# Optimization experiments

Measured on AMD Instinct MI355X. Metric: run time of the kernel, lower is better.

The kernel has to match this reference:

```python
import jax, jax.numpy as jnp
import numpy as np

N = 1024                      # FFT length (init kwarg)
NF = N // 2 + 1               # rfft output length = len(freq)
PB_LO = 40.0 / 60.0           # pulse_band[0] in Hz
PB_HI = 180.0 / 60.0          # pulse_band[1] in Hz
DELTA_HZ = 6.0 / 60.0         # self.delta after /60
W0, W1 = 1.0, 1.0             # weights[0], weights[1]
B, T = 32768, 1024


def setup_inputs() -> dict:
    key = jax.random.key(0)
    k1, k2 = jax.random.split(key)
    preds = jax.random.normal(k1, (B, T), dtype=jnp.float32)
    # realistic camera frame rates ~25-35 Hz (must exceed 2*pulse_band[1]=6 Hz)
    Fs = 25.0 + 10.0 * jax.random.uniform(k2, (B,), dtype=jnp.float32)
    return {"preds": preds, "Fs": Fs}


def reference(preds, Fs):
    idx = jnp.arange(NF)                                            # [Nf]
    # freq = linspace(0, Fs/2, Nf) per sample -> [B, Nf]
    freq = (Fs[:, None] * 0.5) * (idx.astype(jnp.float32) / (NF - 1))
    left = jnp.argmin(jnp.abs(freq - PB_LO), axis=1)                # [B] int
    right = jnp.argmin(jnp.abs(freq - PB_HI), axis=1)               # [B] int

    psd = jnp.abs(jnp.fft.rfft(preds, n=N)) ** 2                    # [B, Nf]
    total = jnp.sum(psd, axis=-1)                                   # [B]

    l = left[:, None]
    r = right[:, None]
    out_band = (idx < l) | (idx >= r)                               # psd[:left] + psd[right:]
    band_loss = jnp.sum(jnp.where(out_band, psd, 0.0), axis=-1) / (1e-8 + total)

    in_band = (idx >= l) & (idx < r)
    # argmax(psd[left:right]) + left  (psd >= 0, so -inf mask is safe)
    peak = jnp.argmax(jnp.where(in_band, psd, -jnp.inf), axis=1)    # [B]
    # delta = max(1, round(self.delta / (Fs/2/len(freq))))  (round half-to-even, as Python)
    delta = jnp.maximum(1.0, jnp.round(DELTA_HZ / (Fs * 0.5 / NF))).astype(jnp.int32)

    p = peak[:, None]
    d = delta[:, None]
    # psd[left:peak-delta] + psd[peak+delta:right]  (empty slices -> 0 via mask)
    sparse_mask = in_band & ((idx < p - d) | (idx >= p + d))
    num = jnp.sum(jnp.where(sparse_mask, psd, 0.0), axis=-1)
    # sum(psd[left:right] + 1e-8) adds 1e-8 per in-band bin, keep faithful
    den = jnp.sum(jnp.where(in_band, psd + 1e-8, 0.0), axis=-1)
    sparse_loss = num / den

    return W0 * jnp.mean(band_loss) + W1 * jnp.mean(sparse_loss)
```

## Files before the change

kernel.cpp:

```cpp
#include <hip/hip_runtime.h>
#include <cmath>

#define BATCH 32768
#define SROW  66

typedef float v2f __attribute__((ext_vector_type(2)));

__device__ __forceinline__ v2f mkc(float r, float i) { v2f t; t.x = r; t.y = i; return t; }
__device__ __forceinline__ v2f cmul(v2f a, v2f b) {
    v2f s = mkc(-a.y, a.x);
    return a * b.x + s * b.y;
}
__device__ __forceinline__ v2f cmul_mi(v2f a){ return mkc(a.y, -a.x); }
__device__ __forceinline__ v2f cmul_w81(v2f a){ const float C=0.70710678f; return mkc(C*(a.x+a.y), C*(a.y-a.x)); }
__device__ __forceinline__ v2f cmul_w83(v2f a){ const float C=0.70710678f; return mkc(C*(a.y-a.x), -C*(a.x+a.y)); }

__device__ __forceinline__ void dft8(v2f a[8]) {
    v2f t0=a[0]+a[4], t4=a[0]-a[4];
    v2f t1=a[1]+a[5], t5=a[1]-a[5];
    v2f t2=a[2]+a[6], t6=a[2]-a[6];
    v2f t3=a[3]+a[7], t7=a[3]-a[7];
    v2f u0=t0+t2, u2=t0-t2;
    v2f u1=t1+t3, u3=cmul_mi(t1-t3);
    a[0]=u0+u1; a[4]=u0-u1; a[2]=u2+u3; a[6]=u2-u3;
    v2f v0=t4, v1=cmul_w81(t5), v2=cmul_mi(t6), v3=cmul_w83(t7);
    v2f w0=v0+v2, w2=v0-v2;
    v2f w1=v1+v3, w3=cmul_mi(v1-v3);
    a[1]=w0+w1; a[5]=w0-w1; a[3]=w2+w3; a[7]=w2-w3;
}

__device__ __forceinline__ float wave_sum64(float x) {
    x += __int_as_float(__builtin_amdgcn_update_dpp(0, __float_as_int(x), 0x111, 0xf, 0xf, true));
    x += __int_as_float(__builtin_amdgcn_update_dpp(0, __float_as_int(x), 0x112, 0xf, 0xf, true));
    x += __int_as_float(__builtin_amdgcn_update_dpp(0, __float_as_int(x), 0x114, 0xf, 0xf, true));
    x += __int_as_float(__builtin_amdgcn_update_dpp(0, __float_as_int(x), 0x118, 0xf, 0xf, true));
    x += __int_as_float(__builtin_amdgcn_update_dpp(0, __float_as_int(x), 0x142, 0xf, 0xf, true));
    x += __int_as_float(__builtin_amdgcn_update_dpp(0, __float_as_int(x), 0x143, 0xf, 0xf, true));
    return __int_as_float(__builtin_amdgcn_readlane(__float_as_int(x), 63));
}
__device__ __forceinline__ int wave_argmax64(float best, int besti) {
#define AM_STEP(ctrl) { \
    float ob = __int_as_float(__builtin_amdgcn_update_dpp(__float_as_int(best), __float_as_int(best), ctrl, 0xf, 0xf, false)); \
    int   oi = __builtin_amdgcn_update_dpp(besti, besti, ctrl, 0xf, 0xf, false); \
    if (ob > best || (ob == best && oi < besti)) { best = ob; besti = oi; } }
    AM_STEP(0x111) AM_STEP(0x112) AM_STEP(0x114) AM_STEP(0x118) AM_STEP(0x142) AM_STEP(0x143)
#undef AM_STEP
    return __builtin_amdgcn_readlane(besti, 63);
}

__device__ __forceinline__ int nearest_bin(float fs, float target) {
    float x = target * 1024.0f / fs;
    int i0 = (int)floorf(x);
    int lo = max(0, i0 - 1), hi = min(512, i0 + 2);
    int bi = lo; float bd = 1e30f;
    for (int i = lo; i <= hi; ++i) {
        float fr = (fs * 0.5f) * ((float)i / 512.0f);
        float d = fabsf(fr - target);
        if (d < bd) { bd = d; bi = i; }
    }
    return bi;
}

__global__ __launch_bounds__(128, 5) void fft_loss_kernel(
    const float* __restrict__ preds, const float* __restrict__ Fs,
    float* __restrict__ wavepartial)
{
    __shared__ v2f lds[2][2][8 * SROW];

    const int tid  = threadIdx.x;
    const int wv   = tid >> 6;
    const int lane = tid & 63;
    const int row0 = blockIdx.x * 4 + wv * 2;

    v2f (*sm)[8 * SROW] = lds[wv];
    const v2f* x2 = reinterpret_cast<const v2f*>(preds) + (size_t)row0 * 512;

    const float fs_[2] = {Fs[row0], Fs[row0 + 1]};
    int left_[2], right_[2];
#pragma unroll
    for (int rr = 0; rr < 2; ++rr) {
        left_[rr]  = nearest_bin(fs_[rr], (float)(40.0 / 60.0));
        right_[rr] = nearest_bin(fs_[rr], 3.0f);
    }

    v2f z[2][8];
    v2f sacc[2]  = {mkc(0.f,0.f), mkc(0.f,0.f)};
    v2f ssacc[2] = {mkc(0.f,0.f), mkc(0.f,0.f)};
#pragma unroll
    for (int rr = 0; rr < 2; ++rr)
#pragma unroll
        for (int n1 = 0; n1 < 8; ++n1) {
            v2f v = x2[rr * 512 + n1 * 64 + lane];
            z[rr][n1] = v;
            sacc[rr]  += v;
            ssacc[rr] += v * v;
        }

    {
        float sb, cb;
        __sincosf(-0.012271846f * (float)lane, &sb, &cb);
        v2f w1 = mkc(cb, sb);
        v2f w2 = cmul(w1, w1), w3 = cmul(w2, w1), w4 = cmul(w2, w2);
        v2f w5 = cmul(w3, w2), w6 = cmul(w3, w3), w7 = cmul(w4, w3);
#pragma unroll
        for (int rr = 0; rr < 2; ++rr) {
            dft8(z[rr]);
            z[rr][1]=cmul(z[rr][1],w1); z[rr][2]=cmul(z[rr][2],w2); z[rr][3]=cmul(z[rr][3],w3);
            z[rr][4]=cmul(z[rr][4],w4); z[rr][5]=cmul(z[rr][5],w5); z[rr][6]=cmul(z[rr][6],w6);
            z[rr][7]=cmul(z[rr][7],w7);
#pragma unroll
            for (int r = 0; r < 8; ++r) sm[rr][r * SROW + lane] = z[rr][r];
        }
    }

    const int rB = lane & 7, m0 = lane >> 3;
    {
        float sb, cb;
        __sincosf(-0.09817477f * (float)m0, &sb, &cb);
        v2f b1 = mkc(cb, sb);
        v2f b2 = cmul(b1, b1), b3 = cmul(b2, b1), b4 = cmul(b2, b2);
        v2f b5 = cmul(b3, b2), b6 = cmul(b3, b3), b7 = cmul(b4, b3);
#pragma unroll
        for (int rr = 0; rr < 2; ++rr) {
#pragma unroll
            for (int m1 = 0; m1 < 8; ++m1) z[rr][m1] = sm[rr][rB * SROW + 8 * m1 + m0];
            dft8(z[rr]);
            z[rr][1]=cmul(z[rr][1],b1); z[rr][2]=cmul(z[rr][2],b2); z[rr][3]=cmul(z[rr][3],b3);
            z[rr][4]=cmul(z[rr][4],b4); z[rr][5]=cmul(z[rr][5],b5); z[rr][6]=cmul(z[rr][6],b6);
            z[rr][7]=cmul(z[rr][7],b7);
#pragma unroll
            for (int s = 0; s < 8; ++s)
                sm[rr][rB * SROW + 8 * m0 + ((s + m0) & 7)] = z[rr][s];
        }
    }

    const int sC = lane >> 3;
#pragma unroll
    for (int rr = 0; rr < 2; ++rr) {
#pragma unroll
        for (int m = 0; m < 8; ++m) z[rr][m] = sm[rr][rB * SROW + 8 * m + ((sC + m) & 7)];
        dft8(z[rr]);
    }

    const int pl = (64 - lane) & 63;
    float wk0x, wk0y;
    {
        float sk, ck;
        __sincosf(-0.0061359233f * (float)lane, &sk, &ck);
        wk0x = ck; wk0y = sk;
    }
    const float W16C = 0.99518473f, W16S = -0.098017140f;

    float acc = 0.f;
#pragma unroll
    for (int rr = 0; rr < 2; ++rr) {
        const int left = left_[rr], right = right_[rr];
        float psd[2];
        float inb = 0.f, best = -1.f;
        int besti = 1 << 30;
#pragma unroll
        for (int t = 0; t < 2; ++t) {
            v2f a = z[rr][t];
            float px = __shfl(z[rr][7 - t].x, pl);
            float py = __shfl(z[rr][7 - t].y, pl);
            if (lane == 0) { px = z[rr][(8 - t) & 7].x; py = z[rr][(8 - t) & 7].y; }
            float wkx = (t == 0) ? wk0x : wk0x * 0.92387953f - wk0y * (-0.38268343f);
            float wky = (t == 0) ? wk0y : wk0x * (-0.38268343f) + wk0y * 0.92387953f;
            float ex = 0.5f * (a.x + px), ey = 0.5f * (a.y - py);
            float dx = a.x - px,          dy = a.y + py;
            float ox = 0.5f * dy,         oy = -0.5f * dx;
            float Xr = ex + wkx * ox - wky * oy;
            float Xi = ey + wkx * oy + wky * ox;
            float v  = Xr * Xr + Xi * Xi;
            psd[t] = v;
            int k = lane + 64 * t;
            if (k >= left && k < right) {
                inb += v;
                if (v > best) { best = v; besti = k; }
            }
        }

        float Se = wave_sum64(sacc[rr].x);
        float So = wave_sum64(sacc[rr].y);
        float SS = wave_sum64(ssacc[rr].x + ssacc[rr].y);
        float X0 = Se + So, X512 = Se - So;
        float total = 0.5f * (1024.0f * SS + X0 * X0 + X512 * X512);

        inb = wave_sum64(inb);
        const int bbi = wave_argmax64(best, besti);

        int delta = (int)rintf(0.1f / ((fs_[rr] * 0.5f) / 513.0f));
        if (delta < 1) delta = 1;
        const int lo = max(left, bbi - delta), hi = min(right, bbi + delta);
        float wsum = 0.f;
#pragma unroll
        for (int t = 0; t < 2; ++t) {
            int k = lane + 64 * t;
            if (k >= lo && k < hi) wsum += psd[t];
        }
        wsum = wave_sum64(wsum);

        float band = (total - inb) / (1e-8f + total);
        float den  = inb + 1e-8f * (float)(right - left);
        acc += band + (inb - wsum) / den;
    }

    if (lane == 0) wavepartial[blockIdx.x * 2 + wv] = acc;
}

__global__ __launch_bounds__(1024) void reduce_kernel(
    const float* __restrict__ wp, float* __restrict__ out)
{
    __shared__ float w[16];
    const int t = threadIdx.x;
    float acc = 0.f;
#pragma unroll
    for (int i = 0; i < 16; ++i) acc += wp[t + 1024 * i];
    acc = wave_sum64(acc);
    const int lane = t & 63, wvi = t >> 6;
    if (lane == 0) w[wvi] = acc;
    __syncthreads();
    if (t == 0) {
        float s = 0.f;
        for (int i = 0; i < 16; ++i) s += w[i];
        out[0] = s * (1.0f / (float)BATCH);
    }
}

extern "C" void kernel_launch(void* const* d_in, const int* in_sizes, int n_in,
                              void* d_out, int out_size, void* d_ws, size_t ws_size,
                              hipStream_t stream) {
    const float* preds = (const float*)d_in[0];
    const float* Fs    = (const float*)d_in[1];
    float* wp          = (float*)d_ws;
    float* out         = (float*)d_out;

    fft_loss_kernel<<<BATCH / 4, 128, 0, stream>>>(preds, Fs, wp);
    reduce_kernel<<<1, 1024, 0, stream>>>(wp, out);
}
```

Before: 194.5 us.

## Process eight rows per wave with register prefetch of the next row

Each wave now loops over eight rows instead of handling two unrolled rows, and issues the next row's global loads into a prefetch buffer before computing the current row's FFT. Twiddles are computed once per wave and reused across rows, and the grid shrinks by a factor of four, so the reduction reads fewer partials. The aim is to hide global-memory latency inside each wave and amortise setup, in exchange for fewer blocks in flight (launch bounds lowered to 4) and a serial per-row dependency.

Result: slower. 219.6 us (+12.9%).

```diff
diff --git a/kernel.cpp b/kernel.cpp
--- a/kernel.cpp
+++ b/kernel.cpp
@@ -3,6 +3,7 @@
 
 #define BATCH 32768
 #define SROW  66
+#define ROWS  8
 
 typedef float v2f __attribute__((ext_vector_type(2)));
 
@@ -61,111 +62,100 @@
     return bi;
 }
 
-__global__ __launch_bounds__(128, 5) void fft_loss_kernel(
+__global__ __launch_bounds__(128, 4) void fft_loss_kernel(
     const float* __restrict__ preds, const float* __restrict__ Fs,
     float* __restrict__ wavepartial)
 {
-    __shared__ v2f lds[2][2][8 * SROW];
+    __shared__ v2f lds[2][8 * SROW];
 
     const int tid  = threadIdx.x;
     const int wv   = tid >> 6;
     const int lane = tid & 63;
-    const int row0 = blockIdx.x * 4 + wv * 2;
-
-    v2f (*sm)[8 * SROW] = lds[wv];
-    const v2f* x2 = reinterpret_cast<const v2f*>(preds) + (size_t)row0 * 512;
-
-    const float fs_[2] = {Fs[row0], Fs[row0 + 1]};
-    int left_[2], right_[2];
-#pragma unroll
-    for (int rr = 0; rr < 2; ++rr) {
-        left_[rr]  = nearest_bin(fs_[rr], (float)(40.0 / 60.0));
-        right_[rr] = nearest_bin(fs_[rr], 3.0f);
-    }
-
-    v2f z[2][8];
-    v2f sacc[2]  = {mkc(0.f,0.f), mkc(0.f,0.f)};
-    v2f ssacc[2] = {mkc(0.f,0.f), mkc(0.f,0.f)};
-#pragma unroll
-    for (int rr = 0; rr < 2; ++rr)
-#pragma unroll
-        for (int n1 = 0; n1 < 8; ++n1) {
-            v2f v = x2[rr * 512 + n1 * 64 + lane];
-            z[rr][n1] = v;
-            sacc[rr]  += v;
-            ssacc[rr] += v * v;
-        }
-
+    const int wave_id = blockIdx.x * 2 + wv;
+    const size_t row0 = (size_t)wave_id * ROWS;
+
+    v2f* sm = lds[wv];
+    const v2f* xbase = reinterpret_cast<const v2f*>(preds) + row0 * 512;
+
+    const int rB = lane & 7, m0 = lane >> 3, sC = lane >> 3;
+    const int pl = (64 - lane) & 63;
+    v2f w1,w2,w3,w4,w5,w6,w7;
     {
-        float sb, cb;
-        __sincosf(-0.012271846f * (float)lane, &sb, &cb);
-        v2f w1 = mkc(cb, sb);
-        v2f w2 = cmul(w1, w1), w3 = cmul(w2, w1), w4 = cmul(w2, w2);
-        v2f w5 = cmul(w3, w2), w6 = cmul(w3, w3), w7 = cmul(w4, w3);
-#pragma unroll
-        for (int rr = 0; rr < 2; ++rr) {
-            dft8(z[rr]);
-            z[rr][1]=cmul(z[rr][1],w1); z[rr][2]=cmul(z[rr][2],w2); z[rr][3]=cmul(z[rr][3],w3);
-            z[rr][4]=cmul(z[rr][4],w4); z[rr][5]=cmul(z[rr][5],w5); z[rr][6]=cmul(z[rr][6],w6);
-            z[rr][7]=cmul(z[rr][7],w7);
-#pragma unroll
-            for (int r = 0; r < 8; ++r) sm[rr][r * SROW + lane] = z[rr][r];
-        }
-    }
-
-    const int rB = lane & 7, m0 = lane >> 3;
+        float sb, cb; __sincosf(-0.012271846f * (float)lane, &sb, &cb);
+        w1 = mkc(cb, sb);
+        w2 = cmul(w1,w1); w3 = cmul(w2,w1); w4 = cmul(w2,w2);
+        w5 = cmul(w3,w2); w6 = cmul(w3,w3); w7 = cmul(w4,w3);
+    }
+    v2f b1,b2,b3,b4,b5,b6,b7;
     {
-        float sb, cb;
-        __sincosf(-0.09817477f * (float)m0, &sb, &cb);
-        v2f b1 = mkc(cb, sb);
-        v2f b2 = cmul(b1, b1), b3 = cmul(b2, b1), b4 = cmul(b2, b2);
-        v2f b5 = cmul(b3, b2), b6 = cmul(b3, b3), b7 = cmul(b4, b3);
-#pragma unroll
-        for (int rr = 0; rr < 2; ++rr) {
-#pragma unroll
-            for (int m1 = 0; m1 < 8; ++m1) z[rr][m1] = sm[rr][rB * SROW + 8 * m1 + m0];
-            dft8(z[rr]);
-            z[rr][1]=cmul(z[rr][1],b1); z[rr][2]=cmul(z[rr][2],b2); z[rr][3]=cmul(z[rr][3],b3);
-            z[rr][4]=cmul(z[rr][4],b4); z[rr][5]=cmul(z[rr][5],b5); z[rr][6]=cmul(z[rr][6],b6);
-            z[rr][7]=cmul(z[rr][7],b7);
-#pragma unroll
-            for (int s = 0; s < 8; ++s)
-                sm[rr][rB * SROW + 8 * m0 + ((s + m0) & 7)] = z[rr][s];
-        }
-    }
-
-    const int sC = lane >> 3;
-#pragma unroll
-    for (int rr = 0; rr < 2; ++rr) {
-#pragma unroll
-        for (int m = 0; m < 8; ++m) z[rr][m] = sm[rr][rB * SROW + 8 * m + ((sC + m) & 7)];
-        dft8(z[rr]);
-    }
-
-    const int pl = (64 - lane) & 63;
-    float wk0x, wk0y;
+        float sb, cb; __sincosf(-0.09817477f * (float)m0, &sb, &cb);
+        b1 = mkc(cb, sb);
+        b2 = cmul(b1,b1); b3 = cmul(b2,b1); b4 = cmul(b2,b2);
+        b5 = cmul(b3,b2); b6 = cmul(b3,b3); b7 = cmul(b4,b3);
+    }
+    float wk0x, wk0y, wk1x, wk1y;
     {
-        float sk, ck;
-        __sincosf(-0.0061359233f * (float)lane, &sk, &ck);
+        float sk, ck; __sincosf(-0.0061359233f * (float)lane, &sk, &ck);
         wk0x = ck; wk0y = sk;
-    }
-    const float W16C = 0.99518473f, W16S = -0.098017140f;
+        wk1x = wk0x * 0.92387953f - wk0y * (-0.38268343f);
+        wk1y = wk0x * (-0.38268343f) + wk0y * 0.92387953f;
+    }
+
+    v2f pre[8];
+    float fs_next = Fs[row0];
+#pragma unroll
+    for (int n1 = 0; n1 < 8; ++n1) pre[n1] = xbase[n1 * 64 + lane];
 
     float acc = 0.f;
-#pragma unroll
-    for (int rr = 0; rr < 2; ++rr) {
-        const int left = left_[rr], right = right_[rr];
+    for (int i = 0; i < ROWS; ++i) {
+        v2f z[8];
+#pragma unroll
+        for (int r = 0; r < 8; ++r) z[r] = pre[r];
+        const float fs = fs_next;
+
+        const int ip = (i + 1 < ROWS) ? i + 1 : i;
+        const v2f* xn = xbase + (size_t)ip * 512;
+        fs_next = Fs[row0 + ip];
+#pragma unroll
+        for (int n1 = 0; n1 < 8; ++n1) pre[n1] = xn[n1 * 64 + lane];
+
+        v2f sacc = mkc(0.f, 0.f), ssacc = mkc(0.f, 0.f);
+#pragma unroll
+        for (int r = 0; r < 8; ++r) { sacc += z[r]; ssacc += z[r] * z[r]; }
+
+        const int left  = nearest_bin(fs, (float)(40.0 / 60.0));
+        const int right = nearest_bin(fs, 3.0f);
+
+        dft8(z);
+        z[1]=cmul(z[1],w1); z[2]=cmul(z[2],w2); z[3]=cmul(z[3],w3);
+        z[4]=cmul(z[4],w4); z[5]=cmul(z[5],w5); z[6]=cmul(z[6],w6); z[7]=cmul(z[7],w7);
+#pragma unroll
+        for (int r = 0; r < 8; ++r) sm[r * SROW + lane] = z[r];
+
+#pragma unroll
+        for (int m1 = 0; m1 < 8; ++m1) z[m1] = sm[rB * SROW + 8 * m1 + m0];
+        dft8(z);
+        z[1]=cmul(z[1],b1); z[2]=cmul(z[2],b2); z[3]=cmul(z[3],b3);
+        z[4]=cmul(z[4],b4); z[5]=cmul(z[5],b5); z[6]=cmul(z[6],b6); z[7]=cmul(z[7],b7);
+#pragma unroll
+        for (int s = 0; s < 8; ++s)
+            sm[rB * SROW + 8 * m0 + ((s + m0) & 7)] = z[s];
+
+#pragma unroll
+        for (int m = 0; m < 8; ++m) z[m] = sm[rB * SROW + 8 * m + ((sC + m) & 7)];
+        dft8(z);
+
         float psd[2];
         float inb = 0.f, best = -1.f;
         int besti = 1 << 30;
 #pragma unroll
         for (int t = 0; t < 2; ++t) {
-            v2f a = z[rr][t];
-            float px = __shfl(z[rr][7 - t].x, pl);
-            float py = __shfl(z[rr][7 - t].y, pl);
-            if (lane == 0) { px = z[rr][(8 - t) & 7].x; py = z[rr][(8 - t) & 7].y; }
-            float wkx = (t == 0) ? wk0x : wk0x * 0.92387953f - wk0y * (-0.38268343f);
-            float wky = (t == 0) ? wk0y : wk0x * (-0.38268343f) + wk0y * 0.92387953f;
+            v2f a = z[t];
+            float px = __shfl(z[7 - t].x, pl);
+            float py = __shfl(z[7 - t].y, pl);
+            if (lane == 0) { px = z[(8 - t) & 7].x; py = z[(8 - t) & 7].y; }
+            float wkx = (t == 0) ? wk0x : wk1x;
+            float wky = (t == 0) ? wk0y : wk1y;
             float ex = 0.5f * (a.x + px), ey = 0.5f * (a.y - py);
             float dx = a.x - px,          dy = a.y + py;
             float ox = 0.5f * dy,         oy = -0.5f * dx;
@@ -180,16 +170,16 @@
             }
         }
 
-        float Se = wave_sum64(sacc[rr].x);
-        float So = wave_sum64(sacc[rr].y);
-        float SS = wave_sum64(ssacc[rr].x + ssacc[rr].y);
+        float Se = wave_sum64(sacc.x);
+        float So = wave_sum64(sacc.y);
+        float SS = wave_sum64(ssacc.x + ssacc.y);
         float X0 = Se + So, X512 = Se - So;
         float total = 0.5f * (1024.0f * SS + X0 * X0 + X512 * X512);
 
         inb = wave_sum64(inb);
         const int bbi = wave_argmax64(best, besti);
 
-        int delta = (int)rintf(0.1f / ((fs_[rr] * 0.5f) / 513.0f));
+        int delta = (int)rintf(0.1f / ((fs * 0.5f) / 513.0f));
         if (delta < 1) delta = 1;
         const int lo = max(left, bbi - delta), hi = min(right, bbi + delta);
         float wsum = 0.f;
@@ -205,7 +195,7 @@
         acc += band + (inb - wsum) / den;
     }
 
-    if (lane == 0) wavepartial[blockIdx.x * 2 + wv] = acc;
+    if (lane == 0) wavepartial[wave_id] = acc;
 }
 
 __global__ __launch_bounds__(1024) void reduce_kernel(
@@ -215,7 +205,7 @@
     const int t = threadIdx.x;
     float acc = 0.f;
 #pragma unroll
-    for (int i = 0; i < 16; ++i) acc += wp[t + 1024 * i];
+    for (int i = 0; i < 4; ++i) acc += wp[t + 1024 * i];
     acc = wave_sum64(acc);
     const int lane = t & 63, wvi = t >> 6;
     if (lane == 0) w[wvi] = acc;
@@ -235,6 +225,6 @@
     float* wp          = (float*)d_ws;
     float* out         = (float*)d_out;
 
-    fft_loss_kernel<<<BATCH / 4, 128, 0, stream>>>(preds, Fs, wp);
+    fft_loss_kernel<<<BATCH / (2 * ROWS), 128, 0, stream>>>(preds, Fs, wp);
     reduce_kernel<<<1, 1024, 0, stream>>>(wp, out);
 }
```
